# Kernel optimization log

Hardware: AMD Instinct MI355X
Metric: run time of the kernel (lower is better)

## Reference

```python
import jax, jax.numpy as jnp
import numpy as np

D = 768
H = 12
HD = D // H
NQ = 100
KV = 257
SEQ = NQ + KV
BS = 32


def layer_norm(x, g, b):
    # torch LayerNorm computed in fp32 then cast back (LayerNorm subclass)
    xf = x.astype(jnp.float32)
    m = xf.mean(-1, keepdims=True)
    v = ((xf - m) ** 2).mean(-1, keepdims=True)
    return ((xf - m) / jnp.sqrt(v + 1e-5) * g + b).astype(x.dtype)


def setup_inputs() -> dict:
    key = jax.random.key(0)
    ks = jax.random.split(key, 8)
    s = 0.02
    return {
        "y": jax.random.normal(ks[0], (SEQ, BS, D), jnp.float32),
        "attn_mask": jax.random.bernoulli(ks[1], 0.3, (BS, NQ, KV)),
        "in_proj_w": jax.random.normal(ks[2], (3 * D, D), jnp.float32) * s,
        "in_proj_b": jnp.zeros((3 * D,), jnp.float32),
        "new_q_w": jax.random.normal(ks[3], (D, D), jnp.float32) * s,
        "new_q_b": jnp.zeros((D,), jnp.float32),
        "out_w": jax.random.normal(ks[4], (D, D), jnp.float32) * s,
        "out_b": jnp.zeros((D,), jnp.float32),
        "ln1_g": jnp.ones((D,), jnp.float32),
        "ln1_b": jnp.zeros((D,), jnp.float32),
        "ln2_g": jnp.ones((D,), jnp.float32),
        "ln2_b": jnp.zeros((D,), jnp.float32),
        "fc_w": jax.random.normal(ks[5], (4 * D, D), jnp.float32) * s,
        "fc_b": jnp.zeros((4 * D,), jnp.float32),
        "proj_w": jax.random.normal(ks[6], (D, 4 * D), jnp.float32) * s,
        "proj_b": jnp.zeros((D,), jnp.float32),
    }


def _attention(x, attn_mask, in_proj_w, in_proj_b, new_q_w, new_q_b, out_w, out_b):
    # x: [seq, bs, D] (already ln_1'd); attn_mask: [bs, nq, kv] bool
    seq, bs, d = x.shape
    nq = attn_mask.shape[1]
    scale = 1.0 / np.sqrt(HD)
    # k/v (and the clip queries) come from the detached non-query tokens
    xkv = jax.lax.stop_gradient(x[nq:])  # [kv, bs, D]
    qkv = xkv @ in_proj_w.T + in_proj_b
    q, k, v = jnp.split(qkv, 3, axis=-1)

    def heads(t):  # [S, bs, D] -> [bs, H, S, hd]
        return t.reshape(t.shape[0], bs, H, HD).transpose(1, 2, 0, 3)

    q = heads(q) * scale
    k = heads(k)
    v = heads(v)
    # regular (clip) attention over shared k/v
    clip_attn = jnp.einsum('bhld,bhmd->bhlm', q, k)
    clip_out = jnp.einsum('bhlm,bhmd->bhld', jax.nn.softmax(clip_attn, axis=-1), v)
    # mask-conditioned queries via new_q_proj (NOT detached)
    new_q = heads(x[:nq] @ new_q_w.T + new_q_b) * scale  # [bs, H, nq, hd]
    bias = jnp.where(attn_mask[:, None], -jnp.inf, 0.0).astype(q.dtype)  # [bs,1,nq,kv]
    mask_attn = jnp.einsum('bhqd,bhmd->bhqm', new_q, k) + bias
    mask_out = jnp.einsum('bhqm,bhmd->bhqd', jax.nn.softmax(mask_attn, axis=-1), v)

    def merge(t):  # [bs, H, S, hd] -> [S, bs, D]
        return t.transpose(2, 0, 1, 3).reshape(t.shape[2], bs, d)

    attn_out = jnp.concatenate([merge(mask_out), merge(clip_out)], axis=0)
    return attn_out @ out_w.T + out_b


def reference(y, attn_mask, in_proj_w, in_proj_b, new_q_w, new_q_b, out_w, out_b,
              ln1_g, ln1_b, ln2_g, ln2_b, fc_w, fc_b, proj_w, proj_b):
    x = layer_norm(y, ln1_g, ln1_b)
    y = y + _attention(x, attn_mask, in_proj_w, in_proj_b, new_q_w, new_q_b, out_w, out_b)
    h = layer_norm(y, ln2_g, ln2_b)
    h = h @ fc_w.T + fc_b
    h = h * jax.nn.sigmoid(1.702 * h)  # QuickGELU
    return y + (h @ proj_w.T + proj_b)
```

## Files before the change

kernel.cpp:

```cpp
#include <hip/hip_runtime.h>


typedef short bf16x8 __attribute__((ext_vector_type(8)));
typedef float f32x4 __attribute__((ext_vector_type(4)));
typedef unsigned short u16;
typedef unsigned long long u64;

__device__ __forceinline__ u16 f2b(float f) {
    unsigned u = __builtin_bit_cast(unsigned, f);
    u = (u + 0x7fffu + ((u >> 16) & 1u)) >> 16;
    return (u16)u;
}
__device__ __forceinline__ float b2f(u16 h) {
    unsigned u = ((unsigned)h) << 16;
    return __builtin_bit_cast(float, u);
}
__device__ __forceinline__ unsigned pack2(float a, float b) {
    return (unsigned)f2b(a) | ((unsigned)f2b(b) << 16);
}
__device__ __forceinline__ void g2l16(const void* g, void* l) {
    __builtin_amdgcn_global_load_lds(
        (__attribute__((address_space(1))) void*)g,
        (__attribute__((address_space(3))) void*)l, 16, 0, 0);
}
#define MFMA16(a, b, c) __builtin_amdgcn_mfma_f32_16x16x32_bf16((a), (b), (c), 0, 0, 0)

__global__ __launch_bounds__(256) void prep_kernel(
    const int* __restrict__ m, u64* __restrict__ mo,
    const float* __restrict__ s0, const float* __restrict__ s1, const float* __restrict__ s2,
    const float* __restrict__ s3, const float* __restrict__ s4, u16* __restrict__ dst)
{
    const int bid = blockIdx.x;
    if (bid < 800) {
        int row = bid * 4 + (threadIdx.x >> 6);
        int lane = threadIdx.x & 63;
        if (row < 3200) {
            const int* r = m + (size_t)row * 257;
            u64 w0 = __ballot(r[lane] != 0);
            u64 w1 = __ballot(r[64 + lane] != 0);
            u64 w2 = __ballot(r[128 + lane] != 0);
            u64 w3 = __ballot(r[192 + lane] != 0);
            u64 w4 = __ballot(lane == 0 && r[256] != 0);
            if (lane == 0) {
                u64* p = mo + (size_t)row * 5;
                p[0] = w0; p[1] = w1; p[2] = w2; p[3] = w3; p[4] = w4;
            }
        }
    }
    int i = bid * 256 + threadIdx.x;
    int stride = gridDim.x * 256;
    for (; i < 1916928; i += stride) {
        const float* src; int off;
        if (i < 442368)       { src = s0; off = i; }
        else if (i < 589824)  { src = s1; off = i - 442368; }
        else if (i < 737280)  { src = s2; off = i - 589824; }
        else if (i < 1327104) { src = s3; off = i - 737280; }
        else                  { src = s4; off = i - 1327104; }
        float4 v = ((const float4*)src)[off];
        ushort4 o;
        o.x = f2b(v.x); o.y = f2b(v.y); o.z = f2b(v.z); o.w = f2b(v.w);
        ((ushort4*)dst)[i] = o;
    }
}

__global__ __launch_bounds__(256) void ln_kernel(
    const float* __restrict__ in, const float* __restrict__ g, const float* __restrict__ be,
    u16* __restrict__ out, int nrows)
{
    int row = blockIdx.x * 4 + (threadIdx.x >> 6);
    int lane = threadIdx.x & 63;
    if (row >= nrows) return;
    const float* p = in + (size_t)row * 768;
    float4 a0 = *(const float4*)(p + lane * 4);
    float4 a1 = *(const float4*)(p + 256 + lane * 4);
    float4 a2 = *(const float4*)(p + 512 + lane * 4);
    float s = a0.x + a0.y + a0.z + a0.w + a1.x + a1.y + a1.z + a1.w + a2.x + a2.y + a2.z + a2.w;
    for (int o = 32; o; o >>= 1) s += __shfl_xor(s, o);
    float mean = s * (1.f / 768.f);
    float vs = 0.f;
#define SQA(t) { float dx; dx = t.x-mean; vs += dx*dx; dx = t.y-mean; vs += dx*dx; dx = t.z-mean; vs += dx*dx; dx = t.w-mean; vs += dx*dx; }
    SQA(a0) SQA(a1) SQA(a2)
#undef SQA
    for (int o = 32; o; o >>= 1) vs += __shfl_xor(vs, o);
    float rstd = rsqrtf(vs * (1.f / 768.f) + 1e-5f);
    u16* orow = out + (size_t)row * 768;
#pragma unroll
    for (int i = 0; i < 3; ++i) {
        int d = i * 256 + lane * 4;
        float4 av = (i == 0) ? a0 : ((i == 1) ? a1 : a2);
        float4 gv = *(const float4*)(g + d);
        float4 bv = *(const float4*)(be + d);
        ushort4 ov;
        ov.x = f2b((av.x - mean) * rstd * gv.x + bv.x);
        ov.y = f2b((av.y - mean) * rstd * gv.y + bv.y);
        ov.z = f2b((av.z - mean) * rstd * gv.z + bv.z);
        ov.w = f2b((av.w - mean) * rstd * gv.w + bv.w);
        *(ushort4*)(orow + d) = ov;
    }
}

template<int ACT, int OUTBF, int RES>
__global__ __launch_bounds__(256) void gemm_bt(
    const u16* __restrict__ A, const u16* __restrict__ B,
    const float* __restrict__ bias, const float* __restrict__ res,
    void* __restrict__ Cp, int M, int N, int K, int G)
{
    __shared__ u16 Al[2][128 * 32];
    __shared__ u16 Bl[2][128 * 32];
    const int t = threadIdx.x;
    const int lane = t & 63, w = t >> 6;
    const int wr = w >> 1, wc = w & 1;
    const int fr = lane & 15, fg = lane >> 4;

    const int raw = blockIdx.x + gridDim.x * blockIdx.y;
    const int rows_per = gridDim.x >> 3;
    const int gy = gridDim.y;
    const int xcd = raw & 7, idx = raw >> 3;
    const int bpg = rows_per * G;
    const int grp = idx / bpg, rem = idx - grp * bpg;
    const int nt = grp * G + rem % G;
    const int mt = xcd * rows_per + rem / G;
    const int m0 = mt * 128, n0 = nt * 128;
    if (m0 >= M) return;

    const int srow = lane >> 2;
    const int scol = (lane & 3) * 8;
    int ar0 = m0 + w * 32 + srow;      int ar1 = ar0 + 16;
    ar0 = ar0 < M ? ar0 : M - 1;       ar1 = ar1 < M ? ar1 : M - 1;
    int br0 = n0 + w * 32 + srow;      int br1 = br0 + 16;
    br0 = br0 < N ? br0 : N - 1;       br1 = br1 < N ? br1 : N - 1;
    const u16* a0p = A + (size_t)ar0 * K + scol;
    const u16* a1p = A + (size_t)ar1 * K + scol;
    const u16* b0p = B + (size_t)br0 * K + scol;
    const u16* b1p = B + (size_t)br1 * K + scol;
    const int lo0 = (w * 2 + 0) * 512, lo1 = (w * 2 + 1) * 512;

    const int nk = K >> 5;
    g2l16(a0p, &Al[0][lo0]);
    g2l16(a1p, &Al[0][lo1]);
    g2l16(b0p, &Bl[0][lo0]);
    g2l16(b1p, &Bl[0][lo1]);
    __syncthreads();

    f32x4 acc[4][4] = {};
#pragma unroll 2
    for (int ki = 0; ki < nk; ++ki) {
        const int cur = ki & 1;
        if (ki + 1 < nk) {
            const int k0 = (ki + 1) << 5;
            const int nxt = cur ^ 1;
            g2l16(a0p + k0, &Al[nxt][lo0]);
            g2l16(a1p + k0, &Al[nxt][lo1]);
            g2l16(b0p + k0, &Bl[nxt][lo0]);
            g2l16(b1p + k0, &Bl[nxt][lo1]);
        }
        bf16x8 af[4], bfr[4];
#pragma unroll
        for (int m = 0; m < 4; ++m) af[m] = *(const bf16x8*)&Al[cur][(wr * 64 + m * 16 + fr) * 32 + fg * 8];
#pragma unroll
        for (int n = 0; n < 4; ++n) bfr[n] = *(const bf16x8*)&Bl[cur][(wc * 64 + n * 16 + fr) * 32 + fg * 8];
#pragma unroll
        for (int m = 0; m < 4; ++m)
#pragma unroll
            for (int n = 0; n < 4; ++n)
                acc[m][n] = MFMA16(af[m], bfr[n], acc[m][n]);
        __syncthreads();
    }
#pragma unroll
    for (int m = 0; m < 4; ++m) {
#pragma unroll
        for (int n = 0; n < 4; ++n) {
            int col = n0 + wc * 64 + n * 16 + fr;
            float bv = bias[col];
#pragma unroll
            for (int r = 0; r < 4; ++r) {
                int row = m0 + wr * 64 + m * 16 + fg * 4 + r;
                if (row < M) {
                    float v = acc[m][n][r] + bv;
                    if (RES) v += res[(size_t)row * N + col];
                    if (ACT) v = v / (1.f + __expf(-1.702f * v));
                    if (OUTBF) ((u16*)Cp)[(size_t)row * N + col] = f2b(v);
                    else       ((float*)Cp)[(size_t)row * N + col] = v;
                }
            }
        }
    }
}

__global__ __launch_bounds__(256, 2) void attn_kernel(
    const u16* __restrict__ qkv,
    const u16* __restrict__ nq,
    const u64* __restrict__ mpk,
    u16* __restrict__ out)
{
    __shared__ u16 Kl[272 * 64];
    __shared__ u16 Vt[64 * 296];
    const int raw = blockIdx.x;
    const int bid = (raw & 7) * 48 + (raw >> 3);
    const int b = bid / 12, h = bid % 12;
    const int t = threadIdx.x, lane = t & 63, wv = t >> 6;
    const int fr = lane & 15, fg = lane >> 4;

    for (int i = t; i < 2048; i += 256) {
        int d = i >> 5, c = 257 + (i & 31);
        if (c < 288) Vt[d * 296 + c] = 0;
    }
    {
        const int r8 = t >> 3, c8 = (t & 7) * 8;
        const u16* kb = qkv + 768 + h * 64 + c8;
        const u16* vb = qkv + 1536 + h * 64 + c8;
#pragma unroll 1
        for (int p = 0; p < 9; ++p) {
            int m = r8 + p * 32;
            if (m <= 256) {
                size_t go = (size_t)(m * 32 + b) * 2304;
                bf16x8 kv = *(const bf16x8*)(kb + go);
                int byte = m * 128 + c8 * 2;
                *(bf16x8*)((char*)Kl + (byte ^ ((m & 7) << 4))) = kv;
                bf16x8 vv = *(const bf16x8*)(vb + go);
#pragma unroll
                for (int j = 0; j < 8; ++j)
                    Vt[(c8 + j) * 296 + m] = (u16)vv[j];
            }
        }
    }
    __syncthreads();

    const int swzK = (fr & 7) << 4;
    const char* KlB = (const char*)Kl;
    const char* VtB = (const char*)Vt;
    const int psrc0 = fr + 32 * (fg & 1);
    const int psrc1 = psrc0 + 16;
    const bool phi = fg >= 2;

    auto fetch = [&](int ti, bf16x8& q0v, bf16x8& q1v, u64* mw, bool& im) {
        int q = ti * 16 + fr;
        int qc = q < 357 ? q : 356;
        im = qc < 100;
        const u16* qp = im ? (nq + (size_t)(qc * 32 + b) * 768 + h * 64)
                           : (qkv + (size_t)((qc - 100) * 32 + b) * 2304 + h * 64);
        q0v = *(const bf16x8*)(qp + fg * 8);
        q1v = *(const bf16x8*)(qp + 32 + fg * 8);
        if (im) {
            const u64* mp = mpk + (size_t)(b * 100 + qc) * 5;
            mw[0] = mp[0]; mw[1] = mp[1]; mw[2] = mp[2]; mw[3] = mp[3]; mw[4] = mp[4];
        } else {
            mw[0] = mw[1] = mw[2] = mw[3] = mw[4] = 0;
        }
    };

    bf16x8 qf0, qf1, qn0, qn1;
    u64 mwc[5], mwn[5];
    bool imc, imn;
    fetch(wv, qf0, qf1, mwc, imc);

#pragma unroll 1
    for (int ti = wv; ti < 23; ti += 4) {
        f32x4 sc[17];
#pragma unroll
        for (int kt = 0; kt < 17; ++kt) {
            int rb = (kt * 16 + fr) * 128;
            bf16x8 ka0 = *(const bf16x8*)(KlB + ((rb + fg * 16) ^ swzK));
            bf16x8 ka1 = *(const bf16x8*)(KlB + ((rb + 64 + fg * 16) ^ swzK));
            f32x4 a = {0.f, 0.f, 0.f, 0.f};
            a = MFMA16(ka0, qf0, a);
            a = MFMA16(ka1, qf1, a);
            sc[kt] = a;
        }
        if (ti + 4 < 23) fetch(ti + 4, qn0, qn1, mwn, imn);
        float tm[17];
#pragma unroll
        for (int kt = 0; kt < 17; ++kt) {
            u64 mw = (kt >> 2) == 0 ? mwc[0] : (kt >> 2) == 1 ? mwc[1] : (kt >> 2) == 2 ? mwc[2]
                   : (kt >> 2) == 3 ? mwc[3] : mwc[4];
            float s0, s1, s2, s3;
            {
                int key = kt * 16 + fg * 4;
                bool b0 = (key > 256) || (imc && ((mw >> (key & 63)) & 1ull));
                bool b1 = (key + 1 > 256) || (imc && ((mw >> ((key + 1) & 63)) & 1ull));
                bool b2 = (key + 2 > 256) || (imc && ((mw >> ((key + 2) & 63)) & 1ull));
                bool b3 = (key + 3 > 256) || (imc && ((mw >> ((key + 3) & 63)) & 1ull));
                s0 = b0 ? -INFINITY : sc[kt][0];
                s1 = b1 ? -INFINITY : sc[kt][1];
                s2 = b2 ? -INFINITY : sc[kt][2];
                s3 = b3 ? -INFINITY : sc[kt][3];
            }
            sc[kt][0] = s0; sc[kt][1] = s1; sc[kt][2] = s2; sc[kt][3] = s3;
            tm[kt] = fmaxf(fmaxf(s0, s1), fmaxf(s2, s3));
        }
        float m8_0 = fmaxf(tm[0], tm[8]),  m8_1 = fmaxf(tm[1], tm[9]);
        float m8_2 = fmaxf(tm[2], tm[10]), m8_3 = fmaxf(tm[3], tm[11]);
        float m8_4 = fmaxf(tm[4], tm[12]), m8_5 = fmaxf(tm[5], tm[13]);
        float m8_6 = fmaxf(tm[6], tm[14]), m8_7 = fmaxf(tm[7], tm[15]);
        float m4_0 = fmaxf(m8_0, m8_4), m4_1 = fmaxf(m8_1, m8_5);
        float m4_2 = fmaxf(m8_2, m8_6), m4_3 = fmaxf(m8_3, m8_7);
        float mx = fmaxf(fmaxf(fmaxf(m4_0, m4_1), fmaxf(m4_2, m4_3)), tm[16]);
        mx = fmaxf(mx, __shfl_xor(mx, 16));
        mx = fmaxf(mx, __shfl_xor(mx, 32));
        float l = 0.f;
        unsigned pk[17][2];
#pragma unroll
        for (int kt = 0; kt < 17; ++kt) {
            float p0 = __expf((sc[kt][0] - mx) * 0.125f);
            float p1 = __expf((sc[kt][1] - mx) * 0.125f);
            float p2 = __expf((sc[kt][2] - mx) * 0.125f);
            float p3 = __expf((sc[kt][3] - mx) * 0.125f);
            l += (p0 + p1) + (p2 + p3);
            pk[kt][0] = pack2(p0, p1);
            pk[kt][1] = pack2(p2, p3);
        }
        l += __shfl_xor(l, 16);
        l += __shfl_xor(l, 32);
        f32x4 oc[4] = {};
#pragma unroll
        for (int c = 0; c < 9; ++c) {
            unsigned p00 = pk[2 * c][0], p01 = pk[2 * c][1];
            unsigned p10 = (c < 8) ? pk[2 * c + 1][0] : 0u;
            unsigned p11 = (c < 8) ? pk[2 * c + 1][1] : 0u;
            unsigned a00 = __shfl(p00, psrc0), a01 = __shfl(p01, psrc0);
            unsigned a10 = __shfl(p10, psrc0), a11 = __shfl(p11, psrc0);
            unsigned b00 = __shfl(p00, psrc1), b01 = __shfl(p01, psrc1);
            unsigned b10 = __shfl(p10, psrc1), b11 = __shfl(p11, psrc1);
            uint4 pw;
            pw.x = phi ? a10 : a00;  pw.y = phi ? a11 : a01;
            pw.z = phi ? b10 : b00;  pw.w = phi ? b11 : b01;
            bf16x8 pf = __builtin_bit_cast(bf16x8, pw);
#pragma unroll
            for (int dt = 0; dt < 4; ++dt) {
                bf16x8 vf = *(const bf16x8*)(VtB + (dt * 16 + fr) * 592 + c * 64 + fg * 16);
                oc[dt] = MFMA16(vf, pf, oc[dt]);
            }
        }
        int q = ti * 16 + fr;
        if (q < 357) {
            float rl = 1.f / l;
            u16* op = out + (size_t)(q * 32 + b) * 768 + h * 64 + fg * 4;
#pragma unroll
            for (int dt = 0; dt < 4; ++dt) {
                ushort4 ov;
                ov.x = f2b(oc[dt][0] * rl); ov.y = f2b(oc[dt][1] * rl);
                ov.z = f2b(oc[dt][2] * rl); ov.w = f2b(oc[dt][3] * rl);
                *(ushort4*)(op + dt * 16) = ov;
            }
        }
        if (ti + 4 < 23) {
            qf0 = qn0; qf1 = qn1; imc = imn;
            mwc[0] = mwn[0]; mwc[1] = mwn[1]; mwc[2] = mwn[2]; mwc[3] = mwn[3]; mwc[4] = mwn[4];
        }
    }
}

extern "C" void kernel_launch(void* const* d_in, const int* in_sizes, int n_in,
                              void* d_out, int out_size, void* d_ws, size_t ws_size,
                              hipStream_t stream)
{
    const float* y   = (const float*)d_in[0];
    const int*   msk = (const int*)  d_in[1];
    const float* ipw = (const float*)d_in[2];
    const float* ipb = (const float*)d_in[3];
    const float* nqw = (const float*)d_in[4];
    const float* nqb = (const float*)d_in[5];
    const float* ow  = (const float*)d_in[6];
    const float* ob  = (const float*)d_in[7];
    const float* l1g = (const float*)d_in[8];
    const float* l1b = (const float*)d_in[9];
    const float* l2g = (const float*)d_in[10];
    const float* l2b = (const float*)d_in[11];
    const float* fcw = (const float*)d_in[12];
    const float* fcb = (const float*)d_in[13];
    const float* pjw = (const float*)d_in[14];
    const float* pjb = (const float*)d_in[15];

    char* ws = (char*)d_ws;
    u16* x_b   = (u16*)(ws + 0);
    u16* qkv_b = (u16*)(ws + 17547264);
    u16* nq_b  = (u16*)(ws + 55443456);
    u16* ao_b  = (u16*)(ws + 60358656);
    u16* h1_b  = (u16*)(ws + 0);
    u16* h_b   = (u16*)(ws + 77905920);
    u64* mpk_b = (u64*)(ws + 77905920);
    u16* w_ip  = (u16*)(ws + 95453184);
    float* out = (float*)d_out;

    prep_kernel<<<2048, 256, 0, stream>>>(msk, mpk_b, ipw, nqw, ow, fcw, pjw, w_ip);

    u16* w_nq  = w_ip + 1769472;
    u16* w_out = w_nq + 589824;
    u16* w_fc  = w_out + 589824;
    u16* w_pj  = w_fc + 2359296;

    ln_kernel<<<2856, 256, 0, stream>>>(y, l1g, l1b, x_b, 11424);
    gemm_bt<0, 1, 0><<<dim3(72, 18), 256, 0, stream>>>(x_b + (size_t)3200 * 768, w_ip, ipb, nullptr, qkv_b, 8224, 2304, 768, 3);
    gemm_bt<0, 1, 0><<<dim3(32, 6), 256, 0, stream>>>(x_b, w_nq, nqb, nullptr, nq_b, 3200, 768, 768, 6);
    attn_kernel<<<384, 256, 0, stream>>>(qkv_b, nq_b, mpk_b, ao_b);
    gemm_bt<0, 0, 1><<<dim3(96, 6), 256, 0, stream>>>(ao_b, w_out, ob, y, out, 11424, 768, 768, 6);
    ln_kernel<<<2856, 256, 0, stream>>>(out, l2g, l2b, h_b, 11424);
    gemm_bt<1, 1, 0><<<dim3(96, 24), 256, 0, stream>>>(h_b, w_fc, fcb, nullptr, h1_b, 11424, 3072, 768, 4);
    gemm_bt<0, 0, 1><<<dim3(96, 6), 256, 0, stream>>>(h1_b, w_pj, pjb, out, out, 11424, 768, 3072, 3);
}
```

Baseline: 431.5 us.

## Merge prep with LN1 and QKV with new-q GEMM into single launches

Combines the weight-cast/mask-pack prep kernel with the first layernorm into one launch, and merges the QKV projection and new_q projection GEMMs into one grid dispatched by block index. It also raises GEMM launch bounds to request 4 blocks per CU. The aim is fewer kernel launches and tail gaps, and letting the smaller GEMM fill idle CUs left by the larger one. The change in register budget could cause spills in the GEMM body.

```diff
diff --git a/kernel.cpp b/kernel.cpp
--- a/kernel.cpp
+++ b/kernel.cpp
@@ -25,51 +25,10 @@
 }
 #define MFMA16(a, b, c) __builtin_amdgcn_mfma_f32_16x16x32_bf16((a), (b), (c), 0, 0, 0)
 
-__global__ __launch_bounds__(256) void prep_kernel(
-    const int* __restrict__ m, u64* __restrict__ mo,
-    const float* __restrict__ s0, const float* __restrict__ s1, const float* __restrict__ s2,
-    const float* __restrict__ s3, const float* __restrict__ s4, u16* __restrict__ dst)
-{
-    const int bid = blockIdx.x;
-    if (bid < 800) {
-        int row = bid * 4 + (threadIdx.x >> 6);
-        int lane = threadIdx.x & 63;
-        if (row < 3200) {
-            const int* r = m + (size_t)row * 257;
-            u64 w0 = __ballot(r[lane] != 0);
-            u64 w1 = __ballot(r[64 + lane] != 0);
-            u64 w2 = __ballot(r[128 + lane] != 0);
-            u64 w3 = __ballot(r[192 + lane] != 0);
-            u64 w4 = __ballot(lane == 0 && r[256] != 0);
-            if (lane == 0) {
-                u64* p = mo + (size_t)row * 5;
-                p[0] = w0; p[1] = w1; p[2] = w2; p[3] = w3; p[4] = w4;
-            }
-        }
-    }
-    int i = bid * 256 + threadIdx.x;
-    int stride = gridDim.x * 256;
-    for (; i < 1916928; i += stride) {
-        const float* src; int off;
-        if (i < 442368)       { src = s0; off = i; }
-        else if (i < 589824)  { src = s1; off = i - 442368; }
-        else if (i < 737280)  { src = s2; off = i - 589824; }
-        else if (i < 1327104) { src = s3; off = i - 737280; }
-        else                  { src = s4; off = i - 1327104; }
-        float4 v = ((const float4*)src)[off];
-        ushort4 o;
-        o.x = f2b(v.x); o.y = f2b(v.y); o.z = f2b(v.z); o.w = f2b(v.w);
-        ((ushort4*)dst)[i] = o;
-    }
-}
-
-__global__ __launch_bounds__(256) void ln_kernel(
+__device__ __forceinline__ void ln_row(
     const float* __restrict__ in, const float* __restrict__ g, const float* __restrict__ be,
-    u16* __restrict__ out, int nrows)
-{
-    int row = blockIdx.x * 4 + (threadIdx.x >> 6);
-    int lane = threadIdx.x & 63;
-    if (row >= nrows) return;
+    u16* __restrict__ out, int row, int lane)
+{
     const float* p = in + (size_t)row * 768;
     float4 a0 = *(const float4*)(p + lane * 4);
     float4 a1 = *(const float4*)(p + 256 + lane * 4);
@@ -99,22 +58,73 @@
     }
 }
 
+__global__ __launch_bounds__(256) void prep_ln(
+    const float* __restrict__ y, const float* __restrict__ l1g, const float* __restrict__ l1b,
+    u16* __restrict__ xb,
+    const int* __restrict__ m, u64* __restrict__ mo,
+    const float* __restrict__ s0, const float* __restrict__ s1, const float* __restrict__ s2,
+    const float* __restrict__ s3, const float* __restrict__ s4, u16* __restrict__ dst)
+{
+    const int bid = blockIdx.x;
+    const int lane = threadIdx.x & 63;
+    if (bid < 2856) {
+        int row = bid * 4 + (threadIdx.x >> 6);
+        if (row < 11424) ln_row(y, l1g, l1b, xb, row, lane);
+        return;
+    }
+    const int cb = bid - 2856;
+    if (cb < 800) {
+        int row = cb * 4 + (threadIdx.x >> 6);
+        if (row < 3200) {
+            const int* r = m + (size_t)row * 257;
+            u64 w0 = __ballot(r[lane] != 0);
+            u64 w1 = __ballot(r[64 + lane] != 0);
+            u64 w2 = __ballot(r[128 + lane] != 0);
+            u64 w3 = __ballot(r[192 + lane] != 0);
+            u64 w4 = __ballot(lane == 0 && r[256] != 0);
+            if (lane == 0) {
+                u64* p = mo + (size_t)row * 5;
+                p[0] = w0; p[1] = w1; p[2] = w2; p[3] = w3; p[4] = w4;
+            }
+        }
+    }
+    int i = cb * 256 + threadIdx.x;
+    const int stride = 2048 * 256;
+    for (; i < 1916928; i += stride) {
+        const float* src; int off;
+        if (i < 442368)       { src = s0; off = i; }
+        else if (i < 589824)  { src = s1; off = i - 442368; }
+        else if (i < 737280)  { src = s2; off = i - 589824; }
+        else if (i < 1327104) { src = s3; off = i - 737280; }
+        else                  { src = s4; off = i - 1327104; }
+        float4 v = ((const float4*)src)[off];
+        ushort4 o;
+        o.x = f2b(v.x); o.y = f2b(v.y); o.z = f2b(v.z); o.w = f2b(v.w);
+        ((ushort4*)dst)[i] = o;
+    }
+}
+
+__global__ __launch_bounds__(256) void ln_kernel(
+    const float* __restrict__ in, const float* __restrict__ g, const float* __restrict__ be,
+    u16* __restrict__ out, int nrows)
+{
+    int row = blockIdx.x * 4 + (threadIdx.x >> 6);
+    if (row < nrows) ln_row(in, g, be, out, row, threadIdx.x & 63);
+}
+
 template<int ACT, int OUTBF, int RES>
-__global__ __launch_bounds__(256) void gemm_bt(
+__device__ __forceinline__ void gemm_body(
+    u16 (*Al)[4096], u16 (*Bl)[4096],
     const u16* __restrict__ A, const u16* __restrict__ B,
     const float* __restrict__ bias, const float* __restrict__ res,
-    void* __restrict__ Cp, int M, int N, int K, int G)
-{
-    __shared__ u16 Al[2][128 * 32];
-    __shared__ u16 Bl[2][128 * 32];
+    void* __restrict__ Cp, int M, int N, int K, int G, int gx, int gy, int raw)
+{
     const int t = threadIdx.x;
     const int lane = t & 63, w = t >> 6;
     const int wr = w >> 1, wc = w & 1;
     const int fr = lane & 15, fg = lane >> 4;
 
-    const int raw = blockIdx.x + gridDim.x * blockIdx.y;
-    const int rows_per = gridDim.x >> 3;
-    const int gy = gridDim.y;
+    const int rows_per = gx >> 3;
     const int xcd = raw & 7, idx = raw >> 3;
     const int bpg = rows_per * G;
     const int grp = idx / bpg, rem = idx - grp * bpg;
@@ -184,6 +194,35 @@
                 }
             }
         }
+    }
+}
+
+template<int ACT, int OUTBF, int RES>
+__global__ __launch_bounds__(256, 4) void gemm_bt(
+    const u16* __restrict__ A, const u16* __restrict__ B,
+    const float* __restrict__ bias, const float* __restrict__ res,
+    void* __restrict__ Cp, int M, int N, int K, int G)
+{
+    __shared__ u16 Al[2][4096];
+    __shared__ u16 Bl[2][4096];
+    const int raw = blockIdx.x + gridDim.x * blockIdx.y;
+    gemm_body<ACT, OUTBF, RES>(Al, Bl, A, B, bias, res, Cp, M, N, K, G,
+                               gridDim.x, gridDim.y, raw);
+}
+
+__global__ __launch_bounds__(256, 4) void gemm_qn(
+    const u16* __restrict__ A0, const u16* __restrict__ B0, const float* __restrict__ b0,
+    u16* __restrict__ C0,
+    const u16* __restrict__ A1, const u16* __restrict__ B1, const float* __restrict__ b1,
+    u16* __restrict__ C1)
+{
+    __shared__ u16 Al[2][4096];
+    __shared__ u16 Bl[2][4096];
+    const int raw = blockIdx.x;
+    if (raw < 1296) {
+        gemm_body<0, 1, 0>(Al, Bl, A0, B0, b0, nullptr, C0, 8224, 2304, 768, 3, 72, 18, raw);
+    } else {
+        gemm_body<0, 1, 0>(Al, Bl, A1, B1, b1, nullptr, C1, 3200, 768, 768, 6, 32, 6, raw - 1296);
     }
 }
 
@@ -382,16 +421,14 @@
     u16* w_ip  = (u16*)(ws + 95453184);
     float* out = (float*)d_out;
 
-    prep_kernel<<<2048, 256, 0, stream>>>(msk, mpk_b, ipw, nqw, ow, fcw, pjw, w_ip);
-
     u16* w_nq  = w_ip + 1769472;
     u16* w_out = w_nq + 589824;
     u16* w_fc  = w_out + 589824;
     u16* w_pj  = w_fc + 2359296;
 
-    ln_kernel<<<2856, 256, 0, stream>>>(y, l1g, l1b, x_b, 11424);
-    gemm_bt<0, 1, 0><<<dim3(72, 18), 256, 0, stream>>>(x_b + (size_t)3200 * 768, w_ip, ipb, nullptr, qkv_b, 8224, 2304, 768, 3);
-    gemm_bt<0, 1, 0><<<dim3(32, 6), 256, 0, stream>>>(x_b, w_nq, nqb, nullptr, nq_b, 3200, 768, 768, 6);
+    prep_ln<<<4904, 256, 0, stream>>>(y, l1g, l1b, x_b, msk, mpk_b, ipw, nqw, ow, fcw, pjw, w_ip);
+    gemm_qn<<<1488, 256, 0, stream>>>(x_b + (size_t)3200 * 768, w_ip, ipb, qkv_b,
+                                      x_b, w_nq, nqb, nq_b);
     attn_kernel<<<384, 256, 0, stream>>>(qkv_b, nq_b, mpk_b, ao_b);
     gemm_bt<0, 0, 1><<<dim3(96, 6), 256, 0, stream>>>(ao_b, w_out, ob, y, out, 11424, 768, 768, 6);
     ln_kernel<<<2856, 256, 0, stream>>>(out, l2g, l2b, h_b, 11424);
```

Measured after the change: 418.8 us (median of 2 runs). 2.9% less time.
